# Optimization experiments

Measured on AMD Instinct MI355X. Metric: run time of the kernel, lower is better.

## Reference

```python
import jax, jax.numpy as jnp
import numpy as np

HEADS = 4
DIM_HEAD = 32
SCALE = DIM_HEAD ** -0.5
GN_EPS = 1e-5


def setup_inputs() -> dict:
    key = jax.random.key(0)
    k1, k2, k3 = jax.random.split(key, 3)
    dim, hidden = 64, HEADS * DIM_HEAD
    x = jax.random.normal(k1, (2, dim, 32, 32, 32), dtype=jnp.float32)
    w_qkv = jax.random.normal(k2, (3 * hidden, dim), dtype=jnp.float32) * (dim ** -0.5)
    w_out = jax.random.normal(k3, (dim, hidden), dtype=jnp.float32) * (hidden ** -0.5)
    b_out = jnp.zeros((dim,), dtype=jnp.float32)
    gn_w = jnp.ones((dim,), dtype=jnp.float32)
    gn_b = jnp.zeros((dim,), dtype=jnp.float32)
    return {"x": x, "w_qkv": w_qkv, "w_out": w_out, "b_out": b_out, "gn_w": gn_w, "gn_b": gn_b}


def reference(x, w_qkv, w_out, b_out, gn_w, gn_b):
    b, c, D, H, W = x.shape
    n = D * H * W
    xf = x.reshape(b, c, n)  # flatten spatial: 1x1 Conv3d == channel matmul
    qkv = jnp.einsum('oc,bcn->bon', w_qkv, xf)  # [b, 3*hidden, n]
    q, k, v = jnp.split(qkv, 3, axis=1)
    rs = lambda t: t.reshape(b, HEADS, DIM_HEAD, n)  # b h d n
    q, k, v = rs(q), rs(k), rs(v)
    q = jax.nn.softmax(q, axis=2) * SCALE   # softmax over head-dim channels
    k = jax.nn.softmax(k, axis=3)           # softmax over spatial positions
    context = jnp.einsum('bhdn,bhen->bhde', k, v)   # [b, h, d, e], tiny
    out = jnp.einsum('bhde,bhdn->bhen', context, q)  # [b, h, e, n]
    out = out.reshape(b, HEADS * DIM_HEAD, n)
    # to_out: 1x1 Conv3d with bias, then GroupNorm(1, dim)
    y = jnp.einsum('oc,bcn->bon', w_out, out) + b_out[None, :, None]
    mean = jnp.mean(y, axis=(1, 2), keepdims=True)
    var = jnp.var(y, axis=(1, 2), keepdims=True)
    y = (y - mean) * jax.lax.rsqrt(var + GN_EPS)
    y = y * gn_w[None, :, None] + gn_b[None, :, None]
    return y.reshape(b, -1, D, H, W)
```

## Files before the change

kernel.cpp:

```cpp
#include <hip/hip_runtime.h>
#include <hip/hip_bf16.h>

#define NB 2
#define C_IN 64
#define N_SP 32768
#define NHEADS 4
#define DH 32
#define HID 128
#define QK_SCALE 0.17677669529663687f
#define GN_EPS_C 1e-5f
#define NGN 2097152.0f

using bf16x8 = __attribute__((ext_vector_type(8))) short;
using f32x4  = __attribute__((ext_vector_type(4))) float;
using u16x4  = __attribute__((ext_vector_type(4))) unsigned short;
using u16x8  = __attribute__((ext_vector_type(8))) unsigned short;

__device__ __forceinline__ unsigned short f2bf(float f) {
    union { float f; unsigned u; } c{f};
    unsigned r = c.u + 0x7FFFu + ((c.u >> 16) & 1u);
    return (unsigned short)(r >> 16);
}
__device__ __forceinline__ float bf2f(unsigned short u) {
    union { unsigned u; float f; } c{ (unsigned)u << 16 };
    return c.f;
}

__device__ __forceinline__ void load_xf(const float* __restrict__ xb, int n0,
        int lg, int lc, bf16x8 xf[2][2]) {
#pragma unroll
    for (int s = 0; s < 2; ++s) {
        int n = n0 + s * 16 + lc;
#pragma unroll
        for (int kk = 0; kk < 2; ++kk) {
            bf16x8 v;
#pragma unroll
            for (int j = 0; j < 8; ++j)
                v[j] = (short)f2bf(xb[(size_t)(kk * 32 + lg * 8 + j) * N_SP + n]);
            xf[s][kk] = v;
        }
    }
}

__global__ __launch_bounds__(512) void kA(const float* __restrict__ x,
        const float* __restrict__ wqkv,
        float* __restrict__ ctx_part, float* __restrict__ ksum_part) {
    __shared__ unsigned short wl[32 * 64 * 8];
    __shared__ unsigned short kt[2][8192];
    __shared__ unsigned short vt[2][8192];
    const int t = threadIdx.x, wv = t >> 6, l = t & 63, lg = l >> 4, lc = l & 15;
    const int blk = blockIdx.x;
    const int b = blk >> 7, nblk = blk & 127;
    const int n0 = nblk * 256 + wv * 32;

#pragma unroll
    for (int i = 0; i < 4; ++i) {
        int idx = t + i * 512;
        int f = idx >> 6, lane = idx & 63;
        int row = (8 + (f >> 1)) * 16 + (lane & 15);
        int c0 = (f & 1) * 32 + (lane >> 4) * 8;
        const float* wp = wqkv + row * 64 + c0;
        u16x8 pk;
#pragma unroll
        for (int j = 0; j < 8; ++j) pk[j] = f2bf(wp[j]);
        *(u16x8*)(wl + (size_t)idx * 8) = pk;
    }

    bf16x8 xf[2][2];
    load_xf(x + (size_t)b * C_IN * N_SP, n0, lg, lc, xf);
    __syncthreads();

    const int di = (wv >> 1) & 1, ei = wv & 1;
#pragma unroll
    for (int h = 0; h < NHEADS; ++h) {
        const int bs = h & 1;
        f32x4 ka[2][2] = {}, va[2][2] = {};
#pragma unroll
        for (int e = 0; e < 2; ++e)
#pragma unroll
            for (int kk = 0; kk < 2; ++kk) {
                bf16x8 wk = *(const bf16x8*)(wl + ((size_t)((2 * h + e) * 2 + kk) * 64 + l) * 8);
                bf16x8 wf = *(const bf16x8*)(wl + ((size_t)(16 + (2 * h + e) * 2 + kk) * 64 + l) * 8);
#pragma unroll
                for (int s = 0; s < 2; ++s) {
                    ka[s][e] = __builtin_amdgcn_mfma_f32_16x16x32_bf16(xf[s][kk], wk, ka[s][e], 0, 0, 0);
                    va[s][e] = __builtin_amdgcn_mfma_f32_16x16x32_bf16(xf[s][kk], wf, va[s][e], 0, 0, 0);
                }
            }
#pragma unroll
        for (int s = 0; s < 2; ++s)
#pragma unroll
            for (int e = 0; e < 2; ++e) {
                u16x4 pk, pv;
#pragma unroll
                for (int r = 0; r < 4; ++r) {
                    pk[r] = f2bf(__expf(ka[s][e][r]));
                    pv[r] = f2bf(va[s][e][r]);
                }
                int ch = e * 16 + lc;
                int pos = wv * 32 + s * 16 + lg * 4;
                int ba = (ch * 512 + pos * 2) ^ ((ch & 7) << 4);
                *(u16x4*)((char*)kt[bs] + ba) = pk;
                *(u16x4*)((char*)vt[bs] + ba) = pv;
            }
        __syncthreads();
        if (wv < 4) {
            f32x4 ca = {};
            float ks = 0.f;
#pragma unroll
            for (int k0 = 0; k0 < 256; k0 += 32) {
                int ar = di * 16 + lc, br = ei * 16 + lc;
                bf16x8 af = *(const bf16x8*)((const char*)kt[bs] + ((ar * 512 + (k0 + lg * 8) * 2) ^ ((ar & 7) << 4)));
                bf16x8 bf = *(const bf16x8*)((const char*)vt[bs] + ((br * 512 + (k0 + lg * 8) * 2) ^ ((br & 7) << 4)));
                if (ei == 0) {
#pragma unroll
                    for (int j = 0; j < 8; ++j) ks += bf2f((unsigned short)af[j]);
                }
                ca = __builtin_amdgcn_mfma_f32_16x16x32_bf16(af, bf, ca, 0, 0, 0);
            }
            float* cp = ctx_part + ((size_t)(b * 4 + h) * 128 + nblk) * 1024;
#pragma unroll
            for (int r = 0; r < 4; ++r)
                cp[(di * 16 + lg * 4 + r) * 32 + ei * 16 + lc] = ca[r];
            if (ei == 0) {
                ks += __shfl_xor(ks, 16);
                ks += __shfl_xor(ks, 32);
                if (lg == 0)
                    ksum_part[((size_t)(b * 4 + h) * 128 + nblk) * 32 + di * 16 + lc] = ks;
            }
        }
    }
}

__global__ __launch_bounds__(256) void kB(const float* __restrict__ ctx_part,
        const float* __restrict__ ksum_part, const float* __restrict__ wout,
        unsigned short* __restrict__ weff) {
    __shared__ float cred2[2][128];
    __shared__ float cred[128];
    __shared__ float ks2[4][32];
    __shared__ float ksl[4];
    const int blk = blockIdx.x;
    const int g = blk >> 3, ds = blk & 7;
    const int bb = g >> 2, h = g & 3;
    const int t = threadIdx.x;
    const int tt = t & 127, th = t >> 7;
    float a = 0.f;
    const float* cp = ctx_part + ((size_t)g * 128 + th * 64) * 1024 + ds * 128 + tt;
#pragma unroll 8
    for (int i = 0; i < 64; ++i) a += cp[(size_t)i * 1024];
    cred2[th][tt] = a;
    if (t < 128) {
        int dl = t >> 5, ic = t & 31;
        float s = 0.f;
        const float* kp = ksum_part + ((size_t)g * 128 + ic * 4) * 32 + ds * 4 + dl;
#pragma unroll
        for (int i = 0; i < 4; ++i) s += kp[i * 32];
        ks2[dl][ic] = s;
    }
    __syncthreads();
    if (t < 128) cred[t] = cred2[0][t] + cred2[1][t];
    if (t < 4) {
        float s = 0.f;
#pragma unroll
        for (int i = 0; i < 32; ++i) s += ks2[t][i];
        ksl[t] = s;
    }
    __syncthreads();
    const int o = t >> 2, dl = t & 3;
    const float* wrow = wout + o * HID + h * 32;
    const float* crow = cred + dl * 32;
    float acc = 0.f;
#pragma unroll
    for (int e = 0; e < 32; ++e) acc = fmaf(wrow[e], crow[e], acc);
    acc /= ksl[dl];
    weff[((size_t)bb * 64 + o) * 128 + h * 32 + ds * 4 + dl] = f2bf(acc);
}

__global__ __launch_bounds__(512) void kC(const float* __restrict__ x,
        const float* __restrict__ wqkv, const unsigned short* __restrict__ weff,
        const float* __restrict__ bout, unsigned short* __restrict__ y_t,
        float* __restrict__ pstats) {
    __shared__ unsigned short wl[16 * 64 * 8];
    __shared__ unsigned short qt[256 * 128];
    __shared__ float red[16];
    const int t = threadIdx.x, wv = t >> 6, l = t & 63, lg = l >> 4, lc = l & 15;
    const int blk = blockIdx.x;
    const int b = blk >> 7, nblk = blk & 127;
    const int n0 = nblk * 256 + wv * 32;

#pragma unroll
    for (int i = 0; i < 2; ++i) {
        int idx = t + i * 512;
        int f = idx >> 6, lane = idx & 63;
        int row = (f >> 1) * 16 + (lane & 15);
        int c0 = (f & 1) * 32 + (lane >> 4) * 8;
        const float* wp = wqkv + row * 64 + c0;
        u16x8 pk;
#pragma unroll
        for (int j = 0; j < 8; ++j) pk[j] = f2bf(wp[j]);
        *(u16x8*)(wl + (size_t)idx * 8) = pk;
    }

    bf16x8 xf[2][2];
    load_xf(x + (size_t)b * C_IN * N_SP, n0, lg, lc, xf);
    __syncthreads();

#pragma unroll
    for (int h = 0; h < NHEADS; ++h) {
        f32x4 qa[2][2] = {};
#pragma unroll
        for (int mi = 0; mi < 2; ++mi)
#pragma unroll
            for (int kk = 0; kk < 2; ++kk) {
                bf16x8 aq = *(const bf16x8*)(wl + ((size_t)((h * 2 + mi) * 2 + kk) * 64 + l) * 8);
#pragma unroll
                for (int s = 0; s < 2; ++s)
                    qa[mi][s] = __builtin_amdgcn_mfma_f32_16x16x32_bf16(aq, xf[s][kk], qa[mi][s], 0, 0, 0);
            }
#pragma unroll
        for (int s = 0; s < 2; ++s) {
            float m = -1e30f;
#pragma unroll
            for (int mi = 0; mi < 2; ++mi)
#pragma unroll
                for (int r = 0; r < 4; ++r) m = fmaxf(m, qa[mi][s][r]);
            m = fmaxf(m, __shfl_xor(m, 16));
            m = fmaxf(m, __shfl_xor(m, 32));
            float sum = 0.f;
#pragma unroll
            for (int mi = 0; mi < 2; ++mi)
#pragma unroll
                for (int r = 0; r < 4; ++r) {
                    float e = __expf(qa[mi][s][r] - m);
                    qa[mi][s][r] = e; sum += e;
                }
            sum += __shfl_xor(sum, 16);
            sum += __shfl_xor(sum, 32);
            float inv = QK_SCALE / sum;
            int pos = wv * 32 + s * 16 + lc;
            int swz = (pos & 7) << 4;
#pragma unroll
            for (int mi = 0; mi < 2; ++mi) {
                u16x4 pk;
#pragma unroll
                for (int r = 0; r < 4; ++r) pk[r] = f2bf(qa[mi][s][r] * inv);
                int ch0 = h * 32 + mi * 16 + lg * 4;
                *(u16x4*)((char*)qt + ((pos * 256 + ch0 * 2) ^ swz)) = pk;
            }
        }
    }

    f32x4 acc[4][2] = {};
    const unsigned short* wb = weff + (size_t)b * 8192;
#pragma unroll
    for (int kk = 0; kk < 4; ++kk) {
        bf16x8 bq[2];
#pragma unroll
        for (int s = 0; s < 2; ++s) {
            int pos = wv * 32 + s * 16 + lc;
            bq[s] = *(const bf16x8*)((const char*)qt +
                ((pos * 256 + (kk * 32 + lg * 8) * 2) ^ ((pos & 7) << 4)));
        }
#pragma unroll
        for (int mt = 0; mt < 4; ++mt) {
            bf16x8 af = *(const bf16x8*)(wb + (size_t)(mt * 16 + lc) * 128 + kk * 32 + lg * 8);
#pragma unroll
            for (int s = 0; s < 2; ++s)
                acc[mt][s] = __builtin_amdgcn_mfma_f32_16x16x32_bf16(af, bq[s], acc[mt][s], 0, 0, 0);
        }
    }
    float s1 = 0.f, s2 = 0.f;
#pragma unroll
    for (int mt = 0; mt < 4; ++mt) {
        float bo[4];
#pragma unroll
        for (int r = 0; r < 4; ++r) bo[r] = bout[mt * 16 + lg * 4 + r];
#pragma unroll
        for (int s = 0; s < 2; ++s) {
            u16x4 pk;
#pragma unroll
            for (int r = 0; r < 4; ++r) {
                float val = acc[mt][s][r] + bo[r];
                s1 += val;
                s2 = fmaf(val, val, s2);
                pk[r] = f2bf(val);
            }
            int n = n0 + s * 16 + lc;
            *(u16x4*)(y_t + ((size_t)b * N_SP + n) * 64 + mt * 16 + lg * 4) = pk;
        }
    }
#pragma unroll
    for (int off = 32; off > 0; off >>= 1) {
        s1 += __shfl_down(s1, off, 64);
        s2 += __shfl_down(s2, off, 64);
    }
    if (l == 0) { red[wv * 2] = s1; red[wv * 2 + 1] = s2; }
    __syncthreads();
    if (t == 0) {
        float S1 = 0.f, S2 = 0.f;
#pragma unroll
        for (int w = 0; w < 8; ++w) { S1 += red[w * 2]; S2 += red[w * 2 + 1]; }
        pstats[(b * 128 + nblk) * 2]     = S1;
        pstats[(b * 128 + nblk) * 2 + 1] = S2;
    }
}

__global__ __launch_bounds__(256) void kE(const unsigned short* __restrict__ y_t,
        const float* __restrict__ pstats, const float* __restrict__ gnw,
        const float* __restrict__ gnb, float* __restrict__ out) {
    __shared__ float red[4];
    __shared__ float ms[2];
    __shared__ float w2s[64], b2s[64];
    const int t = threadIdx.x;
    const int blk = blockIdx.x;
    const int b = blk >> 9, nb = blk & 511;
    float s1 = 0.f, s2 = 0.f;
    if (t < 128) {
        s1 = pstats[(b * 128 + t) * 2];
        s2 = pstats[(b * 128 + t) * 2 + 1];
    }
#pragma unroll
    for (int off = 32; off > 0; off >>= 1) {
        s1 += __shfl_down(s1, off, 64);
        s2 += __shfl_down(s2, off, 64);
    }
    if (t < 128 && (t & 63) == 0) { red[(t >> 6) * 2] = s1; red[(t >> 6) * 2 + 1] = s2; }
    __syncthreads();
    if (t == 0) {
        float S1 = red[0] + red[2], S2 = red[1] + red[3];
        float mean = S1 / NGN;
        float var = S2 / NGN - mean * mean;
        ms[0] = mean; ms[1] = rsqrtf(var + GN_EPS_C);
    }
    __syncthreads();
    if (t < 64) {
        float w2 = gnw[t] * ms[1];
        w2s[t] = w2;
        b2s[t] = gnb[t] - ms[0] * w2;
    }
    __syncthreads();
    const int n = nb * 64 + (t & 63), o0 = (t >> 6) * 16;
    const unsigned short* yp = y_t + ((size_t)b * N_SP + n) * 64 + o0;
    u16x8 v0 = *(const u16x8*)yp;
    u16x8 v1 = *(const u16x8*)(yp + 8);
    float* ob = out + (size_t)b * C_IN * N_SP + n;
#pragma unroll
    for (int j = 0; j < 8; ++j)
        ob[(size_t)(o0 + j) * N_SP] = fmaf(bf2f((unsigned short)v0[j]), w2s[o0 + j], b2s[o0 + j]);
#pragma unroll
    for (int j = 0; j < 8; ++j)
        ob[(size_t)(o0 + 8 + j) * N_SP] = fmaf(bf2f((unsigned short)v1[j]), w2s[o0 + 8 + j], b2s[o0 + 8 + j]);
}

extern "C" void kernel_launch(void* const* d_in, const int* in_sizes, int n_in,
                              void* d_out, int out_size, void* d_ws, size_t ws_size,
                              hipStream_t stream) {
    const float* x    = (const float*)d_in[0];
    const float* wqkv = (const float*)d_in[1];
    const float* wout = (const float*)d_in[2];
    const float* bout = (const float*)d_in[3];
    const float* gnw  = (const float*)d_in[4];
    const float* gnb  = (const float*)d_in[5];
    float* out = (float*)d_out;

    char* ws = (char*)d_ws;
    size_t off = 0;
    float* ctx_part  = (float*)(ws + off); off += (size_t)8 * 128 * 1024 * 4;
    float* ksum_part = (float*)(ws + off); off += (size_t)8 * 128 * 32 * 4;
    unsigned short* weff = (unsigned short*)(ws + off); off += 2 * 8192 * 2;
    unsigned short* y_t  = (unsigned short*)(ws + off); off += (size_t)NB * N_SP * 64 * 2;
    float* pstats = (float*)(ws + off); off += NB * 128 * 2 * 4;

    kA<<<dim3(256), dim3(512), 0, stream>>>(x, wqkv, ctx_part, ksum_part);
    kB<<<dim3(64), dim3(256), 0, stream>>>(ctx_part, ksum_part, wout, weff);
    kC<<<dim3(256), dim3(512), 0, stream>>>(x, wqkv, weff, bout, y_t, pstats);
    kE<<<dim3(1024), dim3(256), 0, stream>>>(y_t, pstats, gnw, gnb, out);
}
```

Before: 42.93 us.

## Fuse four kernels into two using atomic-ticket grid barriers

```diff
diff --git a/kernel.cpp b/kernel.cpp
--- a/kernel.cpp
+++ b/kernel.cpp
@@ -42,12 +42,18 @@
     }
 }
 
-__global__ __launch_bounds__(512) void kA(const float* __restrict__ x,
-        const float* __restrict__ wqkv,
-        float* __restrict__ ctx_part, float* __restrict__ ksum_part) {
+__global__ __launch_bounds__(512, 1) void kAB(const float* __restrict__ x,
+        const float* __restrict__ wqkv, float* __restrict__ ctx_part,
+        float* __restrict__ ksum_part, const float* __restrict__ wout,
+        unsigned short* __restrict__ weff, unsigned int* __restrict__ ctr) {
     __shared__ unsigned short wl[32 * 64 * 8];
     __shared__ unsigned short kt[2][8192];
     __shared__ unsigned short vt[2][8192];
+    __shared__ float cred2[2][128];
+    __shared__ float cred[128];
+    __shared__ float ks2[4][32];
+    __shared__ float ksl[4];
+    __shared__ int tks;
     const int t = threadIdx.x, wv = t >> 6, l = t & 63, lg = l >> 4, lc = l & 15;
     const int blk = blockIdx.x;
     const int b = blk >> 7, nblk = blk & 127;
@@ -130,25 +136,31 @@
             }
         }
     }
-}
-
-__global__ __launch_bounds__(256) void kB(const float* __restrict__ ctx_part,
-        const float* __restrict__ ksum_part, const float* __restrict__ wout,
-        unsigned short* __restrict__ weff) {
-    __shared__ float cred2[2][128];
-    __shared__ float cred[128];
-    __shared__ float ks2[4][32];
-    __shared__ float ksl[4];
-    const int blk = blockIdx.x;
-    const int g = blk >> 3, ds = blk & 7;
+    __syncthreads();
+    if (t == 0) {
+        __threadfence();
+        tks = (int)atomicAdd(ctr, 1u);
+    }
+    __syncthreads();
+    const int ticket = tks;
+    if (ticket < 192) return;
+
+    if (t == 0) {
+        while (atomicAdd(ctr, 0u) < 256u) __builtin_amdgcn_s_sleep(8);
+    }
+    __syncthreads();
+    __threadfence();
+    const int sl = ticket - 192;
+    const int g = sl >> 3, ds = sl & 7;
     const int bb = g >> 2, h = g & 3;
-    const int t = threadIdx.x;
-    const int tt = t & 127, th = t >> 7;
     float a = 0.f;
-    const float* cp = ctx_part + ((size_t)g * 128 + th * 64) * 1024 + ds * 128 + tt;
+    if (t < 256) {
+        const int tt = t & 127, th = t >> 7;
+        const float* cp = ctx_part + ((size_t)g * 128 + th * 64) * 1024 + ds * 128 + tt;
 #pragma unroll 8
-    for (int i = 0; i < 64; ++i) a += cp[(size_t)i * 1024];
-    cred2[th][tt] = a;
+        for (int i = 0; i < 64; ++i) a += cp[(size_t)i * 1024];
+    }
+    if (t < 256) cred2[t >> 7][t & 127] = a;
     if (t < 128) {
         int dl = t >> 5, ic = t & 31;
         float s = 0.f;
@@ -166,23 +178,30 @@
         ksl[t] = s;
     }
     __syncthreads();
-    const int o = t >> 2, dl = t & 3;
-    const float* wrow = wout + o * HID + h * 32;
-    const float* crow = cred + dl * 32;
-    float acc = 0.f;
-#pragma unroll
-    for (int e = 0; e < 32; ++e) acc = fmaf(wrow[e], crow[e], acc);
-    acc /= ksl[dl];
-    weff[((size_t)bb * 64 + o) * 128 + h * 32 + ds * 4 + dl] = f2bf(acc);
-}
-
-__global__ __launch_bounds__(512) void kC(const float* __restrict__ x,
+    if (t < 256) {
+        const int o = t >> 2, dl = t & 3;
+        const float* wrow = wout + o * HID + h * 32;
+        const float* crow = cred + dl * 32;
+        float acc = 0.f;
+#pragma unroll
+        for (int e = 0; e < 32; ++e) acc = fmaf(wrow[e], crow[e], acc);
+        acc /= ksl[dl];
+        weff[((size_t)bb * 64 + o) * 128 + h * 32 + ds * 4 + dl] = f2bf(acc);
+    }
+}
+
+__global__ __launch_bounds__(512, 1) void kCE(const float* __restrict__ x,
         const float* __restrict__ wqkv, const unsigned short* __restrict__ weff,
         const float* __restrict__ bout, unsigned short* __restrict__ y_t,
-        float* __restrict__ pstats) {
+        float* __restrict__ pstats, const float* __restrict__ gnw,
+        const float* __restrict__ gnb, float* __restrict__ out,
+        unsigned int* __restrict__ ctr) {
     __shared__ unsigned short wl[16 * 64 * 8];
     __shared__ unsigned short qt[256 * 128];
     __shared__ float red[16];
+    __shared__ float ms[2];
+    __shared__ float w2s[64], b2s[64];
+    __shared__ int tks;
     const int t = threadIdx.x, wv = t >> 6, l = t & 63, lg = l >> 4, lc = l & 15;
     const int blk = blockIdx.x;
     const int b = blk >> 7, nblk = blk & 127;
@@ -303,28 +322,33 @@
         pstats[(b * 128 + nblk) * 2]     = S1;
         pstats[(b * 128 + nblk) * 2 + 1] = S2;
     }
-}
-
-__global__ __launch_bounds__(256) void kE(const unsigned short* __restrict__ y_t,
-        const float* __restrict__ pstats, const float* __restrict__ gnw,
-        const float* __restrict__ gnb, float* __restrict__ out) {
-    __shared__ float red[4];
-    __shared__ float ms[2];
-    __shared__ float w2s[64], b2s[64];
-    const int t = threadIdx.x;
-    const int blk = blockIdx.x;
-    const int b = blk >> 9, nb = blk & 511;
-    float s1 = 0.f, s2 = 0.f;
+    __syncthreads();
+    if (t == 0) {
+        __threadfence();
+        tks = (int)atomicAdd(ctr, 1u);
+    }
+    __syncthreads();
+    const int ticket = tks;
+    if (ticket < 128) return;
+
+    if (t == 0) {
+        while (atomicAdd(ctr, 0u) < 256u) __builtin_amdgcn_s_sleep(8);
+    }
+    __syncthreads();
+    __threadfence();
+    const int tile0 = (ticket - 128) * 2;
+    const int bb2 = tile0 >> 7;
+    float a1 = 0.f, a2 = 0.f;
     if (t < 128) {
-        s1 = pstats[(b * 128 + t) * 2];
-        s2 = pstats[(b * 128 + t) * 2 + 1];
+        a1 = pstats[(bb2 * 128 + t) * 2];
+        a2 = pstats[(bb2 * 128 + t) * 2 + 1];
     }
 #pragma unroll
     for (int off = 32; off > 0; off >>= 1) {
-        s1 += __shfl_down(s1, off, 64);
-        s2 += __shfl_down(s2, off, 64);
-    }
-    if (t < 128 && (t & 63) == 0) { red[(t >> 6) * 2] = s1; red[(t >> 6) * 2 + 1] = s2; }
+        a1 += __shfl_down(a1, off, 64);
+        a2 += __shfl_down(a2, off, 64);
+    }
+    if (t < 128 && l == 0) { red[(t >> 6) * 2] = a1; red[(t >> 6) * 2 + 1] = a2; }
     __syncthreads();
     if (t == 0) {
         float S1 = red[0] + red[2], S2 = red[1] + red[3];
@@ -339,17 +363,23 @@
         b2s[t] = gnb[t] - ms[0] * w2;
     }
     __syncthreads();
-    const int n = nb * 64 + (t & 63), o0 = (t >> 6) * 16;
-    const unsigned short* yp = y_t + ((size_t)b * N_SP + n) * 64 + o0;
-    u16x8 v0 = *(const u16x8*)yp;
-    u16x8 v1 = *(const u16x8*)(yp + 8);
-    float* ob = out + (size_t)b * C_IN * N_SP + n;
-#pragma unroll
-    for (int j = 0; j < 8; ++j)
-        ob[(size_t)(o0 + j) * N_SP] = fmaf(bf2f((unsigned short)v0[j]), w2s[o0 + j], b2s[o0 + j]);
-#pragma unroll
-    for (int j = 0; j < 8; ++j)
-        ob[(size_t)(o0 + 8 + j) * N_SP] = fmaf(bf2f((unsigned short)v1[j]), w2s[o0 + 8 + j], b2s[o0 + 8 + j]);
+#pragma unroll
+    for (int ti = 0; ti < 2; ++ti) {
+        const int TT = tile0 + ti;
+        const int n = (TT & 127) * 256 + (t & 255);
+        const int o0 = (t >> 8) * 32;
+        const unsigned short* yp = y_t + ((size_t)bb2 * N_SP + n) * 64 + o0;
+        float* ob = out + (size_t)bb2 * C_IN * N_SP + n;
+#pragma unroll
+        for (int q8 = 0; q8 < 4; ++q8) {
+            u16x8 v = *(const u16x8*)(yp + q8 * 8);
+#pragma unroll
+            for (int j = 0; j < 8; ++j) {
+                int o = o0 + q8 * 8 + j;
+                ob[(size_t)o * N_SP] = fmaf(bf2f((unsigned short)v[j]), w2s[o], b2s[o]);
+            }
+        }
+    }
 }
 
 extern "C" void kernel_launch(void* const* d_in, const int* in_sizes, int n_in,
@@ -365,14 +395,14 @@
 
     char* ws = (char*)d_ws;
     size_t off = 0;
+    unsigned int* ctr = (unsigned int*)(ws + off); off += 64;
     float* ctx_part  = (float*)(ws + off); off += (size_t)8 * 128 * 1024 * 4;
     float* ksum_part = (float*)(ws + off); off += (size_t)8 * 128 * 32 * 4;
     unsigned short* weff = (unsigned short*)(ws + off); off += 2 * 8192 * 2;
     unsigned short* y_t  = (unsigned short*)(ws + off); off += (size_t)NB * N_SP * 64 * 2;
     float* pstats = (float*)(ws + off); off += NB * 128 * 2 * 4;
 
-    kA<<<dim3(256), dim3(512), 0, stream>>>(x, wqkv, ctx_part, ksum_part);
-    kB<<<dim3(64), dim3(256), 0, stream>>>(ctx_part, ksum_part, wout, weff);
-    kC<<<dim3(256), dim3(512), 0, stream>>>(x, wqkv, weff, bout, y_t, pstats);
-    kE<<<dim3(1024), dim3(256), 0, stream>>>(y_t, pstats, gnw, gnb, out);
-}
+    hipMemsetAsync(ctr, 0, 64, stream);
+    kAB<<<dim3(256), dim3(512), 0, stream>>>(x, wqkv, ctx_part, ksum_part, wout, weff, ctr + 0);
+    kCE<<<dim3(256), dim3(512), 0, stream>>>(x, wqkv, weff, bout, y_t, pstats, gnw, gnb, out, ctr + 8);
+}
```

Result: slower. 107.4 us (+150.3%).

## Compute Q softmax in first pass and store MFMA-ready bf16 fragments

Applied to the files above, without the earlier changes.

```diff
diff --git a/kernel.cpp b/kernel.cpp
--- a/kernel.cpp
+++ b/kernel.cpp
@@ -43,9 +43,9 @@
 }
 
 __global__ __launch_bounds__(512) void kA(const float* __restrict__ x,
-        const float* __restrict__ wqkv,
+        const float* __restrict__ wqkv, unsigned short* __restrict__ qs_frag,
         float* __restrict__ ctx_part, float* __restrict__ ksum_part) {
-    __shared__ unsigned short wl[32 * 64 * 8];
+    __shared__ unsigned short wl[3072 * 8];
     __shared__ unsigned short kt[2][8192];
     __shared__ unsigned short vt[2][8192];
     const int t = threadIdx.x, wv = t >> 6, l = t & 63, lg = l >> 4, lc = l & 15;
@@ -54,10 +54,10 @@
     const int n0 = nblk * 256 + wv * 32;
 
 #pragma unroll
-    for (int i = 0; i < 4; ++i) {
+    for (int i = 0; i < 6; ++i) {
         int idx = t + i * 512;
         int f = idx >> 6, lane = idx & 63;
-        int row = (8 + (f >> 1)) * 16 + (lane & 15);
+        int row = (f >> 1) * 16 + (lane & 15);
         int c0 = (f & 1) * 32 + (lane >> 4) * 8;
         const float* wp = wqkv + row * 64 + c0;
         u16x8 pk;
@@ -70,6 +70,51 @@
     load_xf(x + (size_t)b * C_IN * N_SP, n0, lg, lc, xf);
     __syncthreads();
 
+#pragma unroll
+    for (int h = 0; h < NHEADS; ++h) {
+        f32x4 qa[2][2] = {};
+#pragma unroll
+        for (int mi = 0; mi < 2; ++mi)
+#pragma unroll
+            for (int kk = 0; kk < 2; ++kk) {
+                bf16x8 aq = *(const bf16x8*)(wl + ((size_t)((h * 2 + mi) * 2 + kk) * 64 + l) * 8);
+#pragma unroll
+                for (int s = 0; s < 2; ++s)
+                    qa[mi][s] = __builtin_amdgcn_mfma_f32_16x16x32_bf16(aq, xf[s][kk], qa[mi][s], 0, 0, 0);
+            }
+#pragma unroll
+        for (int s = 0; s < 2; ++s) {
+            float m = -1e30f;
+#pragma unroll
+            for (int mi = 0; mi < 2; ++mi)
+#pragma unroll
+                for (int r = 0; r < 4; ++r) m = fmaxf(m, qa[mi][s][r]);
+            m = fmaxf(m, __shfl_xor(m, 16));
+            m = fmaxf(m, __shfl_xor(m, 32));
+            float sum = 0.f;
+#pragma unroll
+            for (int mi = 0; mi < 2; ++mi)
+#pragma unroll
+                for (int r = 0; r < 4; ++r) {
+                    float e = __expf(qa[mi][s][r] - m);
+                    qa[mi][s][r] = e; sum += e;
+                }
+            sum += __shfl_xor(sum, 16);
+            sum += __shfl_xor(sum, 32);
+            float inv = QK_SCALE / sum;
+            int pos16 = nblk * 16 + wv * 2 + s;
+            unsigned short* blob = qs_frag + ((size_t)(b * 2048 + pos16) * 4 + h) * 512;
+#pragma unroll
+            for (int mi = 0; mi < 2; ++mi) {
+                u16x4 pk;
+#pragma unroll
+                for (int r = 0; r < 4; ++r) pk[r] = f2bf(qa[mi][s][r] * inv);
+                int lanep = (mi * 2 + (lg >> 1)) * 16 + lc;
+                *(u16x4*)(blob + (size_t)lanep * 8 + (lg & 1) * 4) = pk;
+            }
+        }
+    }
+
     const int di = (wv >> 1) & 1, ei = wv & 1;
 #pragma unroll
     for (int h = 0; h < NHEADS; ++h) {
@@ -79,8 +124,8 @@
         for (int e = 0; e < 2; ++e)
 #pragma unroll
             for (int kk = 0; kk < 2; ++kk) {
-                bf16x8 wk = *(const bf16x8*)(wl + ((size_t)((2 * h + e) * 2 + kk) * 64 + l) * 8);
-                bf16x8 wf = *(const bf16x8*)(wl + ((size_t)(16 + (2 * h + e) * 2 + kk) * 64 + l) * 8);
+                bf16x8 wk = *(const bf16x8*)(wl + ((size_t)((8 + 2 * h + e) * 2 + kk) * 64 + l) * 8);
+                bf16x8 wf = *(const bf16x8*)(wl + ((size_t)((16 + 2 * h + e) * 2 + kk) * 64 + l) * 8);
 #pragma unroll
                 for (int s = 0; s < 2; ++s) {
                     ka[s][e] = __builtin_amdgcn_mfma_f32_16x16x32_bf16(xf[s][kk], wk, ka[s][e], 0, 0, 0);
@@ -176,79 +221,14 @@
     weff[((size_t)bb * 64 + o) * 128 + h * 32 + ds * 4 + dl] = f2bf(acc);
 }
 
-__global__ __launch_bounds__(512) void kC(const float* __restrict__ x,
-        const float* __restrict__ wqkv, const unsigned short* __restrict__ weff,
-        const float* __restrict__ bout, unsigned short* __restrict__ y_t,
-        float* __restrict__ pstats) {
-    __shared__ unsigned short wl[16 * 64 * 8];
-    __shared__ unsigned short qt[256 * 128];
-    __shared__ float red[16];
+__global__ __launch_bounds__(256) void kC(const unsigned short* __restrict__ qs_frag,
+        const unsigned short* __restrict__ weff, const float* __restrict__ bout,
+        unsigned short* __restrict__ y_t, float* __restrict__ pstats) {
+    __shared__ float red[8];
     const int t = threadIdx.x, wv = t >> 6, l = t & 63, lg = l >> 4, lc = l & 15;
     const int blk = blockIdx.x;
-    const int b = blk >> 7, nblk = blk & 127;
-    const int n0 = nblk * 256 + wv * 32;
-
-#pragma unroll
-    for (int i = 0; i < 2; ++i) {
-        int idx = t + i * 512;
-        int f = idx >> 6, lane = idx & 63;
-        int row = (f >> 1) * 16 + (lane & 15);
-        int c0 = (f & 1) * 32 + (lane >> 4) * 8;
-        const float* wp = wqkv + row * 64 + c0;
-        u16x8 pk;
-#pragma unroll
-        for (int j = 0; j < 8; ++j) pk[j] = f2bf(wp[j]);
-        *(u16x8*)(wl + (size_t)idx * 8) = pk;
-    }
-
-    bf16x8 xf[2][2];
-    load_xf(x + (size_t)b * C_IN * N_SP, n0, lg, lc, xf);
-    __syncthreads();
-
-#pragma unroll
-    for (int h = 0; h < NHEADS; ++h) {
-        f32x4 qa[2][2] = {};
-#pragma unroll
-        for (int mi = 0; mi < 2; ++mi)
-#pragma unroll
-            for (int kk = 0; kk < 2; ++kk) {
-                bf16x8 aq = *(const bf16x8*)(wl + ((size_t)((h * 2 + mi) * 2 + kk) * 64 + l) * 8);
-#pragma unroll
-                for (int s = 0; s < 2; ++s)
-                    qa[mi][s] = __builtin_amdgcn_mfma_f32_16x16x32_bf16(aq, xf[s][kk], qa[mi][s], 0, 0, 0);
-            }
-#pragma unroll
-        for (int s = 0; s < 2; ++s) {
-            float m = -1e30f;
-#pragma unroll
-            for (int mi = 0; mi < 2; ++mi)
-#pragma unroll
-                for (int r = 0; r < 4; ++r) m = fmaxf(m, qa[mi][s][r]);
-            m = fmaxf(m, __shfl_xor(m, 16));
-            m = fmaxf(m, __shfl_xor(m, 32));
-            float sum = 0.f;
-#pragma unroll
-            for (int mi = 0; mi < 2; ++mi)
-#pragma unroll
-                for (int r = 0; r < 4; ++r) {
-                    float e = __expf(qa[mi][s][r] - m);
-                    qa[mi][s][r] = e; sum += e;
-                }
-            sum += __shfl_xor(sum, 16);
-            sum += __shfl_xor(sum, 32);
-            float inv = QK_SCALE / sum;
-            int pos = wv * 32 + s * 16 + lc;
-            int swz = (pos & 7) << 4;
-#pragma unroll
-            for (int mi = 0; mi < 2; ++mi) {
-                u16x4 pk;
-#pragma unroll
-                for (int r = 0; r < 4; ++r) pk[r] = f2bf(qa[mi][s][r] * inv);
-                int ch0 = h * 32 + mi * 16 + lg * 4;
-                *(u16x4*)((char*)qt + ((pos * 256 + ch0 * 2) ^ swz)) = pk;
-            }
-        }
-    }
+    const int b = blk >> 8, nblk = blk & 255;
+    const int n0 = nblk * 128 + wv * 32;
 
     f32x4 acc[4][2] = {};
     const unsigned short* wb = weff + (size_t)b * 8192;
@@ -257,9 +237,9 @@
         bf16x8 bq[2];
 #pragma unroll
         for (int s = 0; s < 2; ++s) {
-            int pos = wv * 32 + s * 16 + lc;
-            bq[s] = *(const bf16x8*)((const char*)qt +
-                ((pos * 256 + (kk * 32 + lg * 8) * 2) ^ ((pos & 7) << 4)));
+            int pos16 = nblk * 8 + wv * 2 + s;
+            bq[s] = *(const bf16x8*)(qs_frag +
+                ((size_t)(b * 2048 + pos16) * 4 + kk) * 512 + (size_t)l * 8);
         }
 #pragma unroll
         for (int mt = 0; mt < 4; ++mt) {
@@ -297,37 +277,34 @@
     if (l == 0) { red[wv * 2] = s1; red[wv * 2 + 1] = s2; }
     __syncthreads();
     if (t == 0) {
-        float S1 = 0.f, S2 = 0.f;
-#pragma unroll
-        for (int w = 0; w < 8; ++w) { S1 += red[w * 2]; S2 += red[w * 2 + 1]; }
-        pstats[(b * 128 + nblk) * 2]     = S1;
-        pstats[(b * 128 + nblk) * 2 + 1] = S2;
+        float S1 = red[0] + red[2] + red[4] + red[6];
+        float S2 = red[1] + red[3] + red[5] + red[7];
+        pstats[(b * 256 + nblk) * 2]     = S1;
+        pstats[(b * 256 + nblk) * 2 + 1] = S2;
     }
 }
 
 __global__ __launch_bounds__(256) void kE(const unsigned short* __restrict__ y_t,
         const float* __restrict__ pstats, const float* __restrict__ gnw,
         const float* __restrict__ gnb, float* __restrict__ out) {
-    __shared__ float red[4];
+    __shared__ float red[8];
     __shared__ float ms[2];
     __shared__ float w2s[64], b2s[64];
     const int t = threadIdx.x;
     const int blk = blockIdx.x;
     const int b = blk >> 9, nb = blk & 511;
-    float s1 = 0.f, s2 = 0.f;
-    if (t < 128) {
-        s1 = pstats[(b * 128 + t) * 2];
-        s2 = pstats[(b * 128 + t) * 2 + 1];
-    }
+    float s1 = pstats[(b * 256 + t) * 2];
+    float s2 = pstats[(b * 256 + t) * 2 + 1];
 #pragma unroll
     for (int off = 32; off > 0; off >>= 1) {
         s1 += __shfl_down(s1, off, 64);
         s2 += __shfl_down(s2, off, 64);
     }
-    if (t < 128 && (t & 63) == 0) { red[(t >> 6) * 2] = s1; red[(t >> 6) * 2 + 1] = s2; }
+    if ((t & 63) == 0) { red[(t >> 6) * 2] = s1; red[(t >> 6) * 2 + 1] = s2; }
     __syncthreads();
     if (t == 0) {
-        float S1 = red[0] + red[2], S2 = red[1] + red[3];
+        float S1 = red[0] + red[2] + red[4] + red[6];
+        float S2 = red[1] + red[3] + red[5] + red[7];
         float mean = S1 / NGN;
         float var = S2 / NGN - mean * mean;
         ms[0] = mean; ms[1] = rsqrtf(var + GN_EPS_C);
@@ -365,14 +342,15 @@
 
     char* ws = (char*)d_ws;
     size_t off = 0;
+    unsigned short* qs_frag = (unsigned short*)(ws + off); off += (size_t)NB * 2048 * 4 * 512 * 2;
     float* ctx_part  = (float*)(ws + off); off += (size_t)8 * 128 * 1024 * 4;
     float* ksum_part = (float*)(ws + off); off += (size_t)8 * 128 * 32 * 4;
     unsigned short* weff = (unsigned short*)(ws + off); off += 2 * 8192 * 2;
     unsigned short* y_t  = (unsigned short*)(ws + off); off += (size_t)NB * N_SP * 64 * 2;
-    float* pstats = (float*)(ws + off); off += NB * 128 * 2 * 4;
-
-    kA<<<dim3(256), dim3(512), 0, stream>>>(x, wqkv, ctx_part, ksum_part);
+    float* pstats = (float*)(ws + off); off += NB * 256 * 2 * 4;
+
+    kA<<<dim3(256), dim3(512), 0, stream>>>(x, wqkv, qs_frag, ctx_part, ksum_part);
     kB<<<dim3(64), dim3(256), 0, stream>>>(ctx_part, ksum_part, wout, weff);
-    kC<<<dim3(256), dim3(512), 0, stream>>>(x, wqkv, weff, bout, y_t, pstats);
+    kC<<<dim3(512), dim3(256), 0, stream>>>(qs_frag, weff, bout, y_t, pstats);
     kE<<<dim3(1024), dim3(256), 0, stream>>>(y_t, pstats, gnw, gnb, out);
 }
```

After: 42.95 us. Within noise of the previous version (+0.1%).
